# Kernel optimization log

Measured on AMD Instinct MI355X. Metric: run time of the kernel, lower is better.

## Reference

```python
import jax, jax.numpy as jnp
import numpy as np

B, S, D, H = 2, 2048, 1024, 16
HD = D // H  # head_dim = 64

def setup_inputs() -> dict:
    key = jax.random.key(0)
    ks = jax.random.split(key, 5)
    scale = 0.02
    return {
        "x":  jax.random.normal(ks[0], (B, S, D), dtype=jnp.float32),
        "Wq": jax.random.normal(ks[1], (D, D), dtype=jnp.float32) * scale,
        "Wk": jax.random.normal(ks[2], (D, D), dtype=jnp.float32) * scale,
        "Wv": jax.random.normal(ks[3], (D, D), dtype=jnp.float32) * scale,
        "Wo": jax.random.normal(ks[4], (D, D), dtype=jnp.float32) * scale,
    }

def reference(x, Wq, Wk, Wv, Wo):
    b, s, d = x.shape
    # projections (bias-free linear): [b,s,d] @ [d,d]
    q = (x @ Wq).reshape(b, s, H, HD).transpose(0, 2, 1, 3)  # [b,h,s,hd]
    k = (x @ Wk).reshape(b, s, H, HD).transpose(0, 2, 1, 3)
    v = (x @ Wv).reshape(b, s, H, HD).transpose(0, 2, 1, 3)
    scale = jnp.asarray(1.0 / np.sqrt(HD), dtype=x.dtype)
    scores = jnp.einsum('bhqd,bhkd->bhqk', q, k) * scale  # [b,h,s,s]
    causal = jnp.tril(jnp.ones((s, s), dtype=bool))
    scores = jnp.where(causal, scores, jnp.asarray(-jnp.inf, dtype=scores.dtype))
    attn = jax.nn.softmax(scores, axis=-1)
    out = jnp.einsum('bhqk,bhkd->bhqd', attn, v)  # [b,h,s,hd]
    out = out.transpose(0, 2, 1, 3).reshape(b, s, d)
    return out @ Wo
```

## Files before the change

### kernel.cpp

```cpp
#include <hip/hip_runtime.h>
#include <hip/hip_bf16.h>
#include <cstdint>

typedef __bf16 bf16;
typedef bf16 bf16x8 __attribute__((ext_vector_type(8)));
typedef bf16 bf16x4 __attribute__((ext_vector_type(4)));
typedef float f32x4 __attribute__((ext_vector_type(4)));

#define MFMA16(a, b, c) __builtin_amdgcn_mfma_f32_16x16x32_bf16(a, b, c, 0, 0, 0)

struct rawF { f32x4 a, b; };
__device__ inline rawF ldr(const float* p) {
  rawF r; r.a = *(const f32x4*)p; r.b = *(const f32x4*)(p + 4); return r;
}
__device__ inline bf16x8 ldr(const bf16* p) { return *(const bf16x8*)p; }
__device__ inline bf16x8 cv(const rawF& r) {
  bf16x8 o;
#pragma unroll
  for (int i = 0; i < 4; ++i) { o[i] = (bf16)r.a[i]; o[i + 4] = (bf16)r.b[i]; }
  return o;
}
__device__ inline bf16x8 cv(const bf16x8& r) { return r; }
__device__ inline void stC(bf16* C, size_t i, float v) { C[i] = (bf16)v; }
__device__ inline void stC(float* C, size_t i, float v) { C[i] = v; }

__device__ inline void gl16(const bf16* g, bf16* l) {
  __builtin_amdgcn_global_load_lds(
      (const __attribute__((address_space(1))) void*)g,
      (__attribute__((address_space(3))) void*)l, 16, 0, 0);
}

__device__ inline size_t tile_el(int rowg, int colg) {
  int kq = (colg >> 3) & 3;
  int s = (rowg & 15) ^ kq;
  return ((size_t)(rowg >> 7) * 32 + (colg >> 5)) * 4096 +
         (((rowg >> 6) & 1) << 11) + (((rowg >> 4) & 3) << 9) + (kq << 7) +
         (s << 3) + (colg & 7);
}

__global__ __launch_bounds__(256) void prep_wt(const float* __restrict__ W0,
                                               const float* __restrict__ W1,
                                               const float* __restrict__ W2,
                                               const float* __restrict__ W3,
                                               bf16* __restrict__ Wt, int n) {
  const float* Ws[4] = {W0, W1, W2, W3};
  const float* W = Ws[blockIdx.z];
  bf16* out = Wt + (size_t)blockIdx.z * n * n;
  __shared__ bf16 t[32][33];
  int bx = blockIdx.x * 32, by = blockIdx.y * 32;
  int tx = threadIdx.x & 31, ty = threadIdx.x >> 5;
#pragma unroll
  for (int i = 0; i < 32; i += 8)
    t[ty + i][tx] = (bf16)W[(size_t)(by + ty + i) * n + bx + tx];
  __syncthreads();
#pragma unroll
  for (int i = 0; i < 32; i += 8)
    out[(size_t)(bx + ty + i) * n + by + tx] = t[tx][ty + i];
}

__global__ __launch_bounds__(256) void prep_wt_t(const float* __restrict__ W0,
                                                 const float* __restrict__ W1,
                                                 const float* __restrict__ W2,
                                                 const float* __restrict__ W3,
                                                 bf16* __restrict__ Wt, int n) {
  const float* Ws[4] = {W0, W1, W2, W3};
  const float* W = Ws[blockIdx.z];
  bf16* out = Wt + (size_t)blockIdx.z * n * n;
  __shared__ bf16 t[32][33];
  int bx = blockIdx.x * 32, by = blockIdx.y * 32;
  int tx = threadIdx.x & 31, ty = threadIdx.x >> 5;
#pragma unroll
  for (int i = 0; i < 32; i += 8)
    t[ty + i][tx] = (bf16)W[(size_t)(by + ty + i) * n + bx + tx];
  __syncthreads();
#pragma unroll
  for (int i = 0; i < 32; i += 8) {
    int ng = bx + ty + i, kg = by + tx;
    out[tile_el(ng, kg)] = t[tx][ty + i];
  }
}

__global__ __launch_bounds__(256) void xcvt(const float* __restrict__ x, bf16* __restrict__ Xt) {
  int rbk = blockIdx.x, ks = blockIdx.y, t = threadIdx.x;
  int row = t >> 1, half = t & 1;
  const float* src = x + (size_t)(rbk * 128 + row) * 1024 + ks * 32 + half * 16;
  f32x4 v0 = *(const f32x4*)src;
  f32x4 v1 = *(const f32x4*)(src + 4);
  f32x4 v2 = *(const f32x4*)(src + 8);
  f32x4 v3 = *(const f32x4*)(src + 12);
  bf16* tile = Xt + ((size_t)rbk * 32 + ks) * 4096;
  int rb = (row >> 6) & 1, ii = (row >> 4) & 3;
#pragma unroll
  for (int u = 0; u < 2; ++u) {
    int kq = half * 2 + u;
    int s = (row & 15) ^ kq;
    const f32x4& a = u ? v2 : v0;
    const f32x4& b = u ? v3 : v1;
    bf16x8 o;
#pragma unroll
    for (int j = 0; j < 4; ++j) { o[j] = (bf16)a[j]; o[4 + j] = (bf16)b[j]; }
    *(bf16x8*)&tile[(rb << 11) | (ii << 9) | (kq << 7) | (s << 3)] = o;
  }
}

__global__ __launch_bounds__(256) void vtrans(const bf16* __restrict__ V, bf16* __restrict__ Vt) {
  constexpr int Sn = 2048, Dn = 1024;
  __shared__ bf16 L[64 * 66];
  int s0 = blockIdx.x * 64, bh = blockIdx.y;
  int b = bh >> 4, h = bh & 15;
  int t = threadIdx.x;
  int r = t >> 3, c8 = (t & 7) * 8;
#pragma unroll
  for (int half = 0; half < 2; ++half) {
    int rr = r + half * 32;
    bf16x8 v = *(const bf16x8*)&V[(size_t)(b * Sn + s0 + rr) * Dn + h * 64 + c8];
#pragma unroll
    for (int j = 0; j < 8; ++j) L[(c8 + j) * 66 + rr] = v[j];
  }
  __syncthreads();
  int hd = t >> 3;
#pragma unroll
  for (int half = 0; half < 2; ++half) {
    int hh = hd + half * 32;
    bf16x8 o;
#pragma unroll
    for (int j = 0; j < 8; ++j) o[j] = L[hh * 66 + c8 + j];
    *(bf16x8*)&Vt[(size_t)bh * 64 * Sn + (size_t)hh * Sn + s0 + c8] = o;
  }
}

template <typename TC>
__global__ __launch_bounds__(256) void gemmT(const bf16* __restrict__ At,
                                             const bf16* __restrict__ B0,
                                             const bf16* __restrict__ B1,
                                             const bf16* __restrict__ B2,
                                             TC* __restrict__ C0, TC* __restrict__ C1,
                                             TC* __restrict__ C2, int nsteps, int nblk) {
  __shared__ bf16 As[2][4096];
  __shared__ bf16 Bs[2][4096];
  int tid = threadIdx.x, wave = tid >> 6, lane = tid & 63;
  int la = lane & 15, quad = lane >> 4;
  int by = blockIdx.y, sel = by / nblk, nb = by - sel * nblk;
  const bf16* Bt = sel == 0 ? B0 : (sel == 1 ? B1 : B2);
  TC* C = sel == 0 ? C0 : (sel == 1 ? C1 : C2);
  const bf16* Atb = At + (size_t)blockIdx.x * nsteps * 4096;
  const bf16* Btb = Bt + (size_t)nb * nsteps * 4096;
  int so = wave * 512 + lane * 8;
  int rdA = (wave >> 1) * 2048 + quad * 128 + ((la ^ quad) * 8);
  int rdB = (wave & 1) * 2048 + quad * 128 + ((la ^ quad) * 8);

  f32x4 zero = {0.f, 0.f, 0.f, 0.f};
  f32x4 acc[4][4];
#pragma unroll
  for (int i = 0; i < 4; ++i)
#pragma unroll
    for (int j = 0; j < 4; ++j) acc[i][j] = zero;

  {
    const bf16* ga = Atb;
    const bf16* gb = Btb;
    gl16(ga + so, &As[0][so]);
    gl16(ga + so + 2048, &As[0][so + 2048]);
    gl16(gb + so, &Bs[0][so]);
    gl16(gb + so + 2048, &Bs[0][so + 2048]);
  }
  int cur = 0;
  for (int ks = 0; ks < nsteps; ++ks) {
    __syncthreads();
    if (ks + 1 < nsteps) {
      const bf16* ga = Atb + (size_t)(ks + 1) * 4096;
      const bf16* gb = Btb + (size_t)(ks + 1) * 4096;
      gl16(ga + so, &As[cur ^ 1][so]);
      gl16(ga + so + 2048, &As[cur ^ 1][so + 2048]);
      gl16(gb + so, &Bs[cur ^ 1][so]);
      gl16(gb + so + 2048, &Bs[cur ^ 1][so + 2048]);
    }
    bf16x8 af[4], bfr[4];
#pragma unroll
    for (int i = 0; i < 4; ++i) af[i] = *(const bf16x8*)&As[cur][rdA + i * 512];
#pragma unroll
    for (int j = 0; j < 4; ++j) bfr[j] = *(const bf16x8*)&Bs[cur][rdB + j * 512];
#pragma unroll
    for (int i = 0; i < 4; ++i)
#pragma unroll
      for (int j = 0; j < 4; ++j) acc[i][j] = MFMA16(af[i], bfr[j], acc[i][j]);
    cur ^= 1;
  }
#pragma unroll
  for (int i = 0; i < 4; ++i) {
#pragma unroll
    for (int j = 0; j < 4; ++j) {
      int col = nb * 128 + (wave & 1) * 64 + j * 16 + la;
#pragma unroll
      for (int r = 0; r < 4; ++r) {
        int row = blockIdx.x * 128 + (wave >> 1) * 64 + i * 16 + quad * 4 + r;
        stC(C, (size_t)row * 1024 + col, acc[i][j][r]);
      }
    }
  }
}

template <typename TA, typename TC, bool BT>
__global__ __launch_bounds__(256) void gemm3(const TA* __restrict__ A,
                                             const void* __restrict__ B0p,
                                             const void* __restrict__ B1p,
                                             const void* __restrict__ B2p,
                                             TC* __restrict__ C0, TC* __restrict__ C1,
                                             TC* __restrict__ C2, int M, int N, int K, int nblk) {
  constexpr int LDA = 40;
  __shared__ bf16 As[BT ? 4096 : 5120];
  __shared__ bf16 Bs[4096];
  int tid = threadIdx.x, wave = tid >> 6, lane = tid & 63;
  int la = lane & 15, quad = lane >> 4;
  int wr = (wave >> 1) * 64, wc = (wave & 1) * 64;
  int by = blockIdx.y;
  int sel = by / nblk;
  int n0 = (by - sel * nblk) * 128;
  const void* Bp = sel == 0 ? B0p : (sel == 1 ? B1p : B2p);
  TC* C = sel == 0 ? C0 : (sel == 1 ? C1 : C2);
  const TA* Ab = A + (size_t)blockIdx.x * 128 * K;
  using TB = typename std::conditional<BT, bf16, float>::type;
  const TB* Bm = (const TB*)Bp;

  int ar[2], ac[2], br[2], bc[2], swz[2];
  int sq = tid & 3;
#pragma unroll
  for (int p = 0; p < 2; ++p) {
    int li = (tid + p * 256) * 8;
    ar[p] = li >> 5; ac[p] = li & 31;
    if (BT) { br[p] = li >> 5; bc[p] = li & 31; }
    else    { br[p] = li >> 7; bc[p] = li & 127; }
    int row = ar[p];
    swz[p] = ((row >> 6) << 12) | (((row >> 4) & 3) << 10) | (sq << 8) |
             ((((row & 15) ^ sq)) << 4);
  }
  int rdA = (wave >> 1) * 4096 + quad * 256 + ((la ^ quad) << 4);
  int rdB = (wave & 1) * 4096 + quad * 256 + ((la ^ quad) << 4);

  f32x4 zero = {0.f, 0.f, 0.f, 0.f};
  f32x4 acc[4][4];
#pragma unroll
  for (int i = 0; i < 4; ++i)
#pragma unroll
    for (int j = 0; j < 4; ++j) acc[i][j] = zero;

  decltype(ldr((const TA*)nullptr)) pa[2];
  decltype(ldr((const TB*)nullptr)) pb[2];
#pragma unroll
  for (int p = 0; p < 2; ++p) {
    pa[p] = ldr(&Ab[(size_t)ar[p] * K + ac[p]]);
    if (BT) pb[p] = ldr(&Bm[(size_t)(n0 + br[p]) * K + bc[p]]);
    else    pb[p] = ldr(&Bm[(size_t)br[p] * N + n0 + bc[p]]);
  }

  for (int k0 = 0; k0 < K; k0 += 32) {
#pragma unroll
    for (int p = 0; p < 2; ++p) {
      if constexpr (BT) {
        *(bf16x8*)((char*)As + swz[p]) = cv(pa[p]);
        *(bf16x8*)((char*)Bs + swz[p]) = cv(pb[p]);
      } else {
        *(bf16x8*)&As[ar[p] * LDA + ac[p]] = cv(pa[p]);
        bf16x8 v = cv(pb[p]);
        int kx = br[p] ^ (((bc[p] >> 3) & 3) << 3);
#pragma unroll
        for (int j = 0; j < 8; ++j) Bs[(bc[p] + j) * 32 + kx] = v[j];
      }
    }
    __syncthreads();
    int k1 = k0 + 32;
    if (k1 < K) {
#pragma unroll
      for (int p = 0; p < 2; ++p) {
        pa[p] = ldr(&Ab[(size_t)ar[p] * K + k1 + ac[p]]);
        if (BT) pb[p] = ldr(&Bm[(size_t)(n0 + br[p]) * K + k1 + bc[p]]);
        else    pb[p] = ldr(&Bm[(size_t)(k1 + br[p]) * N + n0 + bc[p]]);
      }
    }
    bf16x8 af[4], bfr[4];
#pragma unroll
    for (int i = 0; i < 4; ++i) {
      if constexpr (BT)
        af[i] = *(const bf16x8*)((const char*)As + rdA + i * 1024);
      else
        af[i] = *(const bf16x8*)&As[(wr + i * 16 + la) * LDA + quad * 8];
    }
#pragma unroll
    for (int j = 0; j < 4; ++j) {
      if constexpr (BT) {
        bfr[j] = *(const bf16x8*)((const char*)Bs + rdB + j * 1024);
      } else {
        int nr = wc + j * 16 + la;
        bfr[j] = *(const bf16x8*)&Bs[nr * 32 + ((quad * 8) ^ (((nr >> 3) & 3) << 3))];
      }
    }
#pragma unroll
    for (int i = 0; i < 4; ++i)
#pragma unroll
      for (int j = 0; j < 4; ++j) acc[i][j] = MFMA16(af[i], bfr[j], acc[i][j]);
    __syncthreads();
  }
#pragma unroll
  for (int i = 0; i < 4; ++i) {
#pragma unroll
    for (int j = 0; j < 4; ++j) {
      int col = n0 + wc + j * 16 + la;
#pragma unroll
      for (int r = 0; r < 4; ++r) {
        int row = blockIdx.x * 128 + wr + i * 16 + quad * 4 + r;
        stC(C, (size_t)row * N + col, acc[i][j][r]);
      }
    }
  }
}

template <bool OT>
__global__ __launch_bounds__(256) void flash_attn(const bf16* __restrict__ Q,
                                                  const bf16* __restrict__ Kg,
                                                  const bf16* __restrict__ Vtg,
                                                  bf16* __restrict__ O,
                                                  bf16* __restrict__ Ot) {
  constexpr int D = 1024, S = 2048;
  const float MASK = -3.0e4f;
  const float SCL2 = 0.18033688011112042f;
  __shared__ bf16 Ks[4096];
  __shared__ bf16 Vs[4096];
  __shared__ bf16 Ps[4096];

  int n = blockIdx.x;
  int bh = n & 31;
  int j5 = n >> 5;
  int j = j5 & 15;
  int qt = (j5 & 16) ? j : 31 - j;
  int b = bh >> 4, h = bh & 15;
  int tid = threadIdx.x, wave = tid >> 6, lane = tid & 63;
  int la = lane & 15, quad = lane >> 4;
  const size_t base = (size_t)b * S * D + (size_t)h * 64;
  const bf16* Qg = Q + base;
  const bf16* Kb = Kg + base;
  const bf16* Vb = Vtg + (size_t)bh * 64 * S;
  int r0 = tid >> 3, c0 = (tid & 7) * 8;

  int quads = (tid & 7) & 3, kcs = (tid & 7) >> 2;
  int st0 = (r0 >> 4) * 1024 + kcs * 512 + quads * 128 +
            (((r0 & 15) ^ quads ^ (kcs << 2)) * 8);
  int kvrd0 = quad * 128 + ((la ^ quad) * 8);
  int kvrd1 = 512 + quad * 128 + ((la ^ quad ^ 4) * 8);
  int prd0 = wave * 1024 + quad * 128 + ((la ^ ((quad & 1) << 2)) * 8);
  int prd1 = prd0 + 512;
  int pwb = wave * 1024 + (quad >> 1) * 128 +
            ((la ^ ((quad >> 1) << 2)) * 8) + (quad & 1) * 4;

  f32x4 zero = {0.f, 0.f, 0.f, 0.f};
  int q0 = qt * 64;
  int ntiles = qt + 1;

  bf16x8 aq[2];
  {
    int qrow = q0 + wave * 16 + la;
#pragma unroll
    for (int kc = 0; kc < 2; ++kc) {
      bf16x8 t = *(const bf16x8*)&Qg[(size_t)qrow * D + kc * 32 + quad * 8];
#pragma unroll
      for (int i = 0; i < 8; ++i) t[i] = (bf16)((float)t[i] * SCL2);
      aq[kc] = t;
    }
  }

  f32x4 o[4];
#pragma unroll
  for (int nt = 0; nt < 4; ++nt) o[nt] = zero;
  float m_l = MASK, l_l = 0.f;

  bf16x8 kr0 = *(const bf16x8*)&Kb[(size_t)r0 * D + c0];
  bf16x8 kr1 = *(const bf16x8*)&Kb[(size_t)(r0 + 32) * D + c0];
  bf16x8 vr0 = *(const bf16x8*)&Vb[(size_t)r0 * S + c0];
  bf16x8 vr1 = *(const bf16x8*)&Vb[(size_t)(r0 + 32) * S + c0];

  for (int t = 0; t < ntiles; ++t) {
    *(bf16x8*)&Ks[st0] = kr0;
    *(bf16x8*)&Ks[st0 + 2048] = kr1;
    *(bf16x8*)&Vs[st0] = vr0;
    *(bf16x8*)&Vs[st0 + 2048] = vr1;
    __syncthreads();
    if (t + 1 < ntiles) {
      int kb2 = (t + 1) * 64;
      kr0 = *(const bf16x8*)&Kb[(size_t)(kb2 + r0) * D + c0];
      kr1 = *(const bf16x8*)&Kb[(size_t)(kb2 + r0 + 32) * D + c0];
      vr0 = *(const bf16x8*)&Vb[(size_t)r0 * S + kb2 + c0];
      vr1 = *(const bf16x8*)&Vb[(size_t)(r0 + 32) * S + kb2 + c0];
    }

    f32x4 s[4];
    __builtin_amdgcn_s_setprio(1);
#pragma unroll
    for (int nt = 0; nt < 4; ++nt) {
      bf16x8 k0f = *(const bf16x8*)&Ks[nt * 1024 + kvrd0];
      bf16x8 k1f = *(const bf16x8*)&Ks[nt * 1024 + kvrd1];
      f32x4 z = zero;
      z = MFMA16(k0f, aq[0], z);
      z = MFMA16(k1f, aq[1], z);
      s[nt] = z;
    }
    __builtin_amdgcn_s_setprio(0);

    if (t == qt) {
      int qa = q0 + wave * 16 + la;
      int kb = t * 64;
#pragma unroll
      for (int nt = 0; nt < 4; ++nt)
#pragma unroll
        for (int r = 0; r < 4; ++r) {
          int ka = kb + nt * 16 + quad * 4 + r;
          s[nt][r] = (ka > qa) ? MASK : s[nt][r];
        }
    }

    float mx;
    {
      float u0 = fmaxf(fmaxf(s[0][0], s[0][1]), fmaxf(s[0][2], s[0][3]));
      float u1 = fmaxf(fmaxf(s[1][0], s[1][1]), fmaxf(s[1][2], s[1][3]));
      float u2 = fmaxf(fmaxf(s[2][0], s[2][1]), fmaxf(s[2][2], s[2][3]));
      float u3 = fmaxf(fmaxf(s[3][0], s[3][1]), fmaxf(s[3][2], s[3][3]));
      mx = fmaxf(fmaxf(u0, u1), fmaxf(u2, u3));
    }
    mx = fmaxf(mx, m_l);
    mx = fmaxf(mx, __shfl_xor(mx, 16, 64));
    mx = fmaxf(mx, __shfl_xor(mx, 32, 64));

    if (!__all(mx - m_l <= 8.0f)) {
      float alpha = __builtin_amdgcn_exp2f(m_l - mx);
      m_l = mx;
      l_l *= alpha;
      float ab[4];
#pragma unroll
      for (int r = 0; r < 4; ++r) ab[r] = __shfl(alpha, quad * 4 + r, 64);
#pragma unroll
      for (int nt = 0; nt < 4; ++nt)
#pragma unroll
        for (int r = 0; r < 4; ++r) o[nt][r] *= ab[r];
    }

    float rs = 0.f;
#pragma unroll
    for (int nt = 0; nt < 4; ++nt) {
      float p0 = __builtin_amdgcn_exp2f(s[nt][0] - m_l);
      float p1 = __builtin_amdgcn_exp2f(s[nt][1] - m_l);
      float p2 = __builtin_amdgcn_exp2f(s[nt][2] - m_l);
      float p3 = __builtin_amdgcn_exp2f(s[nt][3] - m_l);
      s[nt][0] = p0; s[nt][1] = p1; s[nt][2] = p2; s[nt][3] = p3;
      rs += (p0 + p1) + (p2 + p3);
    }
    rs += __shfl_xor(rs, 16, 64);
    rs += __shfl_xor(rs, 32, 64);
    l_l += rs;

#pragma unroll
    for (int nt = 0; nt < 4; ++nt) {
      bf16x4 pk;
#pragma unroll
      for (int r = 0; r < 4; ++r) pk[r] = (bf16)s[nt][r];
      *(bf16x4*)&Ps[pwb + nt * 256] = pk;
    }

    __builtin_amdgcn_s_setprio(1);
    {
      bf16x8 ap0 = *(const bf16x8*)&Ps[prd0];
#pragma unroll
      for (int nt = 0; nt < 4; ++nt) {
        bf16x8 bv = *(const bf16x8*)&Vs[nt * 1024 + kvrd0];
        o[nt] = MFMA16(ap0, bv, o[nt]);
      }
      bf16x8 ap1 = *(const bf16x8*)&Ps[prd1];
#pragma unroll
      for (int nt = 0; nt < 4; ++nt) {
        bf16x8 bv = *(const bf16x8*)&Vs[nt * 1024 + kvrd1];
        o[nt] = MFMA16(ap1, bv, o[nt]);
      }
    }
    __builtin_amdgcn_s_setprio(0);
    __syncthreads();
  }

  float inv[4];
#pragma unroll
  for (int r = 0; r < 4; ++r) {
    float lv = __shfl(l_l, quad * 4 + r, 64);
    inv[r] = (lv > 1e-30f) ? 1.0f / lv : 0.0f;
  }
#pragma unroll
  for (int nt = 0; nt < 4; ++nt) {
    int hd = nt * 16 + la;
#pragma unroll
    for (int r = 0; r < 4; ++r) {
      int row = q0 + wave * 16 + quad * 4 + r;
      float v = o[nt][r] * inv[r];
      if (OT) {
        int rowg = b * S + row, colg = h * 64 + hd;
        Ot[tile_el(rowg, colg)] = (bf16)v;
      } else {
        O[base + (size_t)row * D + hd] = (bf16)v;
      }
    }
  }
}

extern "C" void kernel_launch(void* const* d_in, const int* in_sizes, int n_in,
                              void* d_out, int out_size, void* d_ws, size_t ws_size,
                              hipStream_t stream) {
  constexpr int B = 2, S = 2048, D = 1024;
  constexpr int M = B * S;
  constexpr size_t WN = (size_t)D * D;
  constexpr size_t XN = (size_t)M * D;

  const float* x = (const float*)d_in[0];
  const float* Wq = (const float*)d_in[1];
  const float* Wk = (const float*)d_in[2];
  const float* Wv = (const float*)d_in[3];
  const float* Wo = (const float*)d_in[4];
  float* out = (float*)d_out;

  if (ws_size < 2 * XN * sizeof(bf16)) return;
  bf16* Qb = (bf16*)d_ws;
  bf16* Vtg = Qb + XN;
  bf16* Wt = Vtg + XN;
  bf16* Xt = Wt + 4 * WN;
  bf16* Kb = (bf16*)d_out;
  bf16* Vb = Kb + XN;
  bool use_bt = ws_size >= (2 * XN + 4 * WN) * sizeof(bf16);
  bool big_ws = ws_size >= (3 * XN + 4 * WN) * sizeof(bf16);

  if (big_ws) {
    prep_wt_t<<<dim3(32, 32, 4), 256, 0, stream>>>(Wq, Wk, Wv, Wo, Wt, D);
    xcvt<<<dim3(32, 32), 256, 0, stream>>>(x, Xt);
    gemmT<bf16><<<dim3(M / 128, 24), 256, 0, stream>>>(Xt, Wt, Wt + WN, Wt + 2 * WN,
                                                       Qb, Kb, Vb, 32, 8);
    vtrans<<<dim3(S / 64, 32), 256, 0, stream>>>(Vb, Vtg);
    flash_attn<true><<<dim3(1024), 256, 0, stream>>>(Qb, Kb, Vtg, nullptr, Xt);
    gemmT<float><<<dim3(M / 128, 8), 256, 0, stream>>>(Xt, Wt + 3 * WN, Wt + 3 * WN,
                                                       Wt + 3 * WN, out, out, out, 32, 8);
    return;
  }

  dim3 gq(M / 128, 24), gf(M / 128, 8);
  if (use_bt) {
    prep_wt<<<dim3(32, 32, 4), 256, 0, stream>>>(Wq, Wk, Wv, Wo, Wt, D);
    gemm3<float, bf16, true><<<gq, 256, 0, stream>>>(x, Wt, Wt + WN, Wt + 2 * WN,
                                                     Qb, Kb, Vb, M, D, D, 8);
  } else {
    gemm3<float, bf16, false><<<gq, 256, 0, stream>>>(x, Wq, Wk, Wv, Qb, Kb, Vb, M, D, D, 8);
  }
  vtrans<<<dim3(S / 64, 32), 256, 0, stream>>>(Vb, Vtg);
  flash_attn<false><<<dim3(1024), 256, 0, stream>>>(Qb, Kb, Vtg, Qb, nullptr);
  if (use_bt) {
    gemm3<bf16, float, true><<<gf, 256, 0, stream>>>(Qb, Wt + 3 * WN, Wt + 3 * WN, Wt + 3 * WN,
                                                     out, out, out, M, D, D, 8);
  } else {
    gemm3<bf16, float, false><<<gf, 256, 0, stream>>>(Qb, Wo, Wo, Wo, out, out, out, M, D, D, 8);
  }
}
```

Measured before the change: 176.7 us.

## Drop x pre-tiling pass; use gemm3 for QKV and tiled layout only for Wo

The big-workspace path no longer runs the separate xcvt kernel that converted x into a pre-tiled bf16 layout. The QKV projection goes back to gemm3, which reads fp32 x directly and converts it on the fly. Only Wo is still pre-tiled (prep_wt_t now writes vectorised 8-element stores), and the output GEMM keeps the tiled gemmT path with a simplified signature. Flash attention's rescale and normalise steps are rewritten as f32x4 vector multiplies. This saves one kernel launch and one pass over x, at the cost of a QKV GEMM that may load less efficiently.

```diff
diff --git a/kernel.cpp b/kernel.cpp
--- a/kernel.cpp
+++ b/kernel.cpp
@@ -58,14 +58,8 @@
     out[(size_t)(bx + ty + i) * n + by + tx] = t[tx][ty + i];
 }
 
-__global__ __launch_bounds__(256) void prep_wt_t(const float* __restrict__ W0,
-                                                 const float* __restrict__ W1,
-                                                 const float* __restrict__ W2,
-                                                 const float* __restrict__ W3,
-                                                 bf16* __restrict__ Wt, int n) {
-  const float* Ws[4] = {W0, W1, W2, W3};
-  const float* W = Ws[blockIdx.z];
-  bf16* out = Wt + (size_t)blockIdx.z * n * n;
+__global__ __launch_bounds__(256) void prep_wt_t(const float* __restrict__ W,
+                                                 bf16* __restrict__ out, int n) {
   __shared__ bf16 t[32][33];
   int bx = blockIdx.x * 32, by = blockIdx.y * 32;
   int tx = threadIdx.x & 31, ty = threadIdx.x >> 5;
@@ -73,33 +67,13 @@
   for (int i = 0; i < 32; i += 8)
     t[ty + i][tx] = (bf16)W[(size_t)(by + ty + i) * n + bx + tx];
   __syncthreads();
-#pragma unroll
-  for (int i = 0; i < 32; i += 8) {
-    int ng = bx + ty + i, kg = by + tx;
-    out[tile_el(ng, kg)] = t[tx][ty + i];
-  }
-}
-
-__global__ __launch_bounds__(256) void xcvt(const float* __restrict__ x, bf16* __restrict__ Xt) {
-  int rbk = blockIdx.x, ks = blockIdx.y, t = threadIdx.x;
-  int row = t >> 1, half = t & 1;
-  const float* src = x + (size_t)(rbk * 128 + row) * 1024 + ks * 32 + half * 16;
-  f32x4 v0 = *(const f32x4*)src;
-  f32x4 v1 = *(const f32x4*)(src + 4);
-  f32x4 v2 = *(const f32x4*)(src + 8);
-  f32x4 v3 = *(const f32x4*)(src + 12);
-  bf16* tile = Xt + ((size_t)rbk * 32 + ks) * 4096;
-  int rb = (row >> 6) & 1, ii = (row >> 4) & 3;
-#pragma unroll
-  for (int u = 0; u < 2; ++u) {
-    int kq = half * 2 + u;
-    int s = (row & 15) ^ kq;
-    const f32x4& a = u ? v2 : v0;
-    const f32x4& b = u ? v3 : v1;
+  int tid = threadIdx.x;
+  if (tid < 128) {
+    int ngl = tid >> 2, kc0 = (tid & 3) * 8;
     bf16x8 o;
 #pragma unroll
-    for (int j = 0; j < 4; ++j) { o[j] = (bf16)a[j]; o[4 + j] = (bf16)b[j]; }
-    *(bf16x8*)&tile[(rb << 11) | (ii << 9) | (kq << 7) | (s << 3)] = o;
+    for (int j = 0; j < 8; ++j) o[j] = t[kc0 + j][ngl];
+    *(bf16x8*)&out[tile_el(bx + ngl, by + kc0)] = o;
   }
 }
 
@@ -131,18 +105,13 @@
 
 template <typename TC>
 __global__ __launch_bounds__(256) void gemmT(const bf16* __restrict__ At,
-                                             const bf16* __restrict__ B0,
-                                             const bf16* __restrict__ B1,
-                                             const bf16* __restrict__ B2,
-                                             TC* __restrict__ C0, TC* __restrict__ C1,
-                                             TC* __restrict__ C2, int nsteps, int nblk) {
+                                             const bf16* __restrict__ Bt,
+                                             TC* __restrict__ C, int nsteps) {
   __shared__ bf16 As[2][4096];
   __shared__ bf16 Bs[2][4096];
   int tid = threadIdx.x, wave = tid >> 6, lane = tid & 63;
   int la = lane & 15, quad = lane >> 4;
-  int by = blockIdx.y, sel = by / nblk, nb = by - sel * nblk;
-  const bf16* Bt = sel == 0 ? B0 : (sel == 1 ? B1 : B2);
-  TC* C = sel == 0 ? C0 : (sel == 1 ? C1 : C2);
+  int nb = blockIdx.y;
   const bf16* Atb = At + (size_t)blockIdx.x * nsteps * 4096;
   const bf16* Btb = Bt + (size_t)nb * nsteps * 4096;
   int so = wave * 512 + lane * 8;
@@ -156,14 +125,11 @@
 #pragma unroll
     for (int j = 0; j < 4; ++j) acc[i][j] = zero;
 
-  {
-    const bf16* ga = Atb;
-    const bf16* gb = Btb;
-    gl16(ga + so, &As[0][so]);
-    gl16(ga + so + 2048, &As[0][so + 2048]);
-    gl16(gb + so, &Bs[0][so]);
-    gl16(gb + so + 2048, &Bs[0][so + 2048]);
-  }
+  gl16(Atb + so, &As[0][so]);
+  gl16(Atb + so + 2048, &As[0][so + 2048]);
+  gl16(Btb + so, &Bs[0][so]);
+  gl16(Btb + so + 2048, &Bs[0][so + 2048]);
+
   int cur = 0;
   for (int ks = 0; ks < nsteps; ++ks) {
     __syncthreads();
@@ -432,22 +398,22 @@
       float alpha = __builtin_amdgcn_exp2f(m_l - mx);
       m_l = mx;
       l_l *= alpha;
-      float ab[4];
-#pragma unroll
-      for (int r = 0; r < 4; ++r) ab[r] = __shfl(alpha, quad * 4 + r, 64);
-#pragma unroll
-      for (int nt = 0; nt < 4; ++nt)
-#pragma unroll
-        for (int r = 0; r < 4; ++r) o[nt][r] *= ab[r];
-    }
-
+      f32x4 abv;
+#pragma unroll
+      for (int r = 0; r < 4; ++r) abv[r] = __shfl(alpha, quad * 4 + r, 64);
+#pragma unroll
+      for (int nt = 0; nt < 4; ++nt) o[nt] *= abv;
+    }
+
+    f32x4 mlv = {m_l, m_l, m_l, m_l};
     float rs = 0.f;
 #pragma unroll
     for (int nt = 0; nt < 4; ++nt) {
-      float p0 = __builtin_amdgcn_exp2f(s[nt][0] - m_l);
-      float p1 = __builtin_amdgcn_exp2f(s[nt][1] - m_l);
-      float p2 = __builtin_amdgcn_exp2f(s[nt][2] - m_l);
-      float p3 = __builtin_amdgcn_exp2f(s[nt][3] - m_l);
+      f32x4 d = s[nt] - mlv;
+      float p0 = __builtin_amdgcn_exp2f(d[0]);
+      float p1 = __builtin_amdgcn_exp2f(d[1]);
+      float p2 = __builtin_amdgcn_exp2f(d[2]);
+      float p3 = __builtin_amdgcn_exp2f(d[3]);
       s[nt][0] = p0; s[nt][1] = p1; s[nt][2] = p2; s[nt][3] = p3;
       rs += (p0 + p1) + (p2 + p3);
     }
@@ -482,24 +448,24 @@
     __syncthreads();
   }
 
-  float inv[4];
+  f32x4 invv;
 #pragma unroll
   for (int r = 0; r < 4; ++r) {
     float lv = __shfl(l_l, quad * 4 + r, 64);
-    inv[r] = (lv > 1e-30f) ? 1.0f / lv : 0.0f;
+    invv[r] = (lv > 1e-30f) ? 1.0f / lv : 0.0f;
   }
 #pragma unroll
   for (int nt = 0; nt < 4; ++nt) {
+    o[nt] *= invv;
     int hd = nt * 16 + la;
 #pragma unroll
     for (int r = 0; r < 4; ++r) {
       int row = q0 + wave * 16 + quad * 4 + r;
-      float v = o[nt][r] * inv[r];
       if (OT) {
         int rowg = b * S + row, colg = h * 64 + hd;
-        Ot[tile_el(rowg, colg)] = (bf16)v;
+        Ot[tile_el(rowg, colg)] = (bf16)o[nt][r];
       } else {
-        O[base + (size_t)row * D + hd] = (bf16)v;
+        O[base + (size_t)row * D + hd] = (bf16)o[nt][r];
       }
     }
   }
@@ -524,25 +490,24 @@
   bf16* Qb = (bf16*)d_ws;
   bf16* Vtg = Qb + XN;
   bf16* Wt = Vtg + XN;
-  bf16* Xt = Wt + 4 * WN;
+  bf16* Ot = Wt + 4 * WN;
   bf16* Kb = (bf16*)d_out;
   bf16* Vb = Kb + XN;
   bool use_bt = ws_size >= (2 * XN + 4 * WN) * sizeof(bf16);
   bool big_ws = ws_size >= (3 * XN + 4 * WN) * sizeof(bf16);
 
+  dim3 gq(M / 128, 24), gf(M / 128, 8);
   if (big_ws) {
-    prep_wt_t<<<dim3(32, 32, 4), 256, 0, stream>>>(Wq, Wk, Wv, Wo, Wt, D);
-    xcvt<<<dim3(32, 32), 256, 0, stream>>>(x, Xt);
-    gemmT<bf16><<<dim3(M / 128, 24), 256, 0, stream>>>(Xt, Wt, Wt + WN, Wt + 2 * WN,
-                                                       Qb, Kb, Vb, 32, 8);
+    prep_wt<<<dim3(32, 32, 3), 256, 0, stream>>>(Wq, Wk, Wv, Wq, Wt, D);
+    prep_wt_t<<<dim3(32, 32), 256, 0, stream>>>(Wo, Wt + 3 * WN, D);
+    gemm3<float, bf16, true><<<gq, 256, 0, stream>>>(x, Wt, Wt + WN, Wt + 2 * WN,
+                                                     Qb, Kb, Vb, M, D, D, 8);
     vtrans<<<dim3(S / 64, 32), 256, 0, stream>>>(Vb, Vtg);
-    flash_attn<true><<<dim3(1024), 256, 0, stream>>>(Qb, Kb, Vtg, nullptr, Xt);
-    gemmT<float><<<dim3(M / 128, 8), 256, 0, stream>>>(Xt, Wt + 3 * WN, Wt + 3 * WN,
-                                                       Wt + 3 * WN, out, out, out, 32, 8);
+    flash_attn<true><<<dim3(1024), 256, 0, stream>>>(Qb, Kb, Vtg, nullptr, Ot);
+    gemmT<float><<<gf, 256, 0, stream>>>(Ot, Wt + 3 * WN, out, 32);
     return;
   }
 
-  dim3 gq(M / 128, 24), gf(M / 128, 8);
   if (use_bt) {
     prep_wt<<<dim3(32, 32, 4), 256, 0, stream>>>(Wq, Wk, Wv, Wo, Wt, D);
     gemm3<float, bf16, true><<<gq, 256, 0, stream>>>(x, Wt, Wt + WN, Wt + 2 * WN,
```

New measurement: 183.1 us. 3.6% more time.
